# Optimization experiments

Hardware: AMD Instinct MI355X
Metric: run time of the kernel (lower is better)

Reference implementation:

```python
import jax, jax.numpy as jnp
import numpy as np
from jax import lax

CLIP = 5.0
LN_EPS = 1e-5


def _embed(feats, mean, std, W, b, g, beta):
    # InputNorm (eval mode, count>1): normalize with running stats, clamp.
    h = jnp.clip((feats - mean) / std, -CLIP, CLIP)
    h = lax.stop_gradient(h)  # torch runs InputNorm under no_grad
    # Linear + ReLU
    h = jax.nn.relu(h @ W + b)
    # LayerNorm over d_model
    mu = h.mean(-1, keepdims=True)
    var = ((h - mu) ** 2).mean(-1, keepdims=True)
    return (h - mu) / jnp.sqrt(var + LN_EPS) * g + beta


def setup_inputs() -> dict:
    key = jax.random.key(0)
    ks = jax.random.split(key, 8)
    nA, fA = 300000, 32
    nB, fB = 150000, 48
    d = 256
    B = 512
    inp = {
        "featsA": jax.random.normal(ks[0], (nA, fA), jnp.float32),
        "featsB": jax.random.normal(ks[1], (nB, fB), jnp.float32),
        "normA_mean": jnp.zeros((fA,), jnp.float32),
        "normA_std": jnp.ones((fA,), jnp.float32),
        "normB_mean": jnp.zeros((fB,), jnp.float32),
        "normB_std": jnp.ones((fB,), jnp.float32),
        "WA": jax.random.normal(ks[2], (fA, d), jnp.float32) / np.sqrt(fA),
        "bA": jnp.zeros((d,), jnp.float32),
        "lnA_g": jnp.ones((d,), jnp.float32),
        "lnA_b": jnp.zeros((d,), jnp.float32),
        "WB_": jax.random.normal(ks[3], (fB, d), jnp.float32) / np.sqrt(fB),
        "bB": jnp.zeros((d,), jnp.float32),
        "lnB_g": jnp.ones((d,), jnp.float32),
        "lnB_b": jnp.zeros((d,), jnp.float32),
        "Wback": jax.random.normal(ks[4], (d, d), jnp.float32) / np.sqrt(d),
        "bback": jnp.zeros((d,), jnp.float32),
        "Wv": jax.random.normal(ks[5], (d, 1), jnp.float32) / np.sqrt(d),
        "bv": jnp.zeros((1,), jnp.float32),
        "batch_index": jax.random.randint(ks[6], (nA + nB,), 0, B, jnp.int64)
        if jax.config.jax_enable_x64 else jax.random.randint(ks[6], (nA + nB,), 0, B, jnp.int32).astype(jnp.int32),
        "num_obs": B,
    }
    return inp


def reference(featsA, featsB, normA_mean, normA_std, normB_mean, normB_std,
              WA, bA, lnA_g, lnA_b, WB_, bB, lnB_g, lnB_b,
              Wback, bback, Wv, bv, batch_index, num_obs):
    # Per-entity-type embedding stacks, concatenated in entity-type order
    xA = _embed(featsA, normA_mean, normA_std, WA, bA, lnA_g, lnA_b)
    xB = _embed(featsB, normB_mean, normB_std, WB_, bB, lnB_g, lnB_b)
    x = jnp.concatenate([xA, xB], axis=0)          # [N, d]
    x = jax.nn.relu(x @ Wback + bback)              # backbone
    # torch_scatter mean pooling over observations
    sums = jax.ops.segment_sum(x, batch_index, num_segments=num_obs)
    counts = jax.ops.segment_sum(jnp.ones((x.shape[0],), x.dtype), batch_index,
                                 num_segments=num_obs)
    pooled = sums / jnp.maximum(counts, 1.0)[:, None]  # empty segments -> 0
    return pooled @ Wv + bv                          # [num_obs, 1]
```

## Files before the change

kernel.cpp:

```cpp
#include <hip/hip_runtime.h>

#define NSEG 512
#define NSPLIT 32

typedef __attribute__((ext_vector_type(8))) short short8;
typedef __attribute__((ext_vector_type(4))) short short4v;
typedef __attribute__((ext_vector_type(4))) float floatx4;

#define WS_WAT   0
#define WS_WBT2  16384
#define WS_W2GA  49152
#define WS_W2GB  180224
#define WS_C1A   311296
#define WS_C2A   312320
#define WS_C1B   313344
#define WS_C2B   314368
#define WS_INVA  315392
#define WS_INVB  315520
#define WS_VPART 315712
#define WS_CPART 381248

__device__ __forceinline__ short f2bf(float f) {
  unsigned u = __builtin_bit_cast(unsigned, f);
  u += 0x7FFFu + ((u >> 16) & 1u);
  return (short)(u >> 16);
}

__global__ void prep_kernel(const float* __restrict__ WA, const float* __restrict__ WB,
                            const float* __restrict__ Wback,
                            const float* __restrict__ gA, const float* __restrict__ betaA,
                            const float* __restrict__ gB, const float* __restrict__ betaB,
                            const float* __restrict__ bback,
                            const float* __restrict__ sA, const float* __restrict__ sB,
                            char* __restrict__ ws) {
  short* waT  = (short*)(ws + WS_WAT);
  short* wbT2 = (short*)(ws + WS_WBT2);
  short* w2gA = (short*)(ws + WS_W2GA);
  short* w2gB = (short*)(ws + WS_W2GB);
  float* c1A = (float*)(ws + WS_C1A);
  float* c2A = (float*)(ws + WS_C2A);
  float* c1B = (float*)(ws + WS_C1B);
  float* c2B = (float*)(ws + WS_C2B);
  float* invA = (float*)(ws + WS_INVA);
  float* invB = (float*)(ws + WS_INVB);
  float* vz   = (float*)(ws + WS_VPART);
  int tid = blockIdx.x * blockDim.x + threadIdx.x;
  int stride = gridDim.x * blockDim.x;
  for (int i = tid; i < 32*256; i += stride) {
    int n = i >> 5, k = i & 31;
    waT[i] = f2bf(WA[k*256 + n]);
  }
  for (int i = tid; i < 256*64; i += stride) {
    int n = i >> 6, k = i & 63;
    wbT2[i] = (k < 48) ? f2bf(WB[k*256 + n]) : (short)0;
  }
  for (int i = tid; i < 256*256; i += stride) {
    int n = i >> 8, k = i & 255;
    float w = Wback[k*256 + n];
    w2gA[i] = f2bf(gA[k] * w);
    w2gB[i] = f2bf(gB[k] * w);
  }
  if (blockIdx.x < 4 && threadIdx.x < 256) {
    int n = threadIdx.x;
    int which = blockIdx.x;
    const float* coef = (which == 0) ? gA : (which == 1) ? betaA : (which == 2) ? gB : betaB;
    float a = 0.f;
    #pragma unroll 8
    for (int k = 0; k < 256; k++) a = fmaf(coef[k], Wback[k*256 + n], a);
    if (which == 0)      c1A[n] = a;
    else if (which == 1) c2A[n] = a + bback[n];
    else if (which == 2) c1B[n] = a;
    else                 c2B[n] = a + bback[n];
  }
  if (tid < 32) invA[tid] = 1.0f / sA[tid];
  if (tid < 48) invB[tid] = 1.0f / sB[tid];
  for (int i = tid; i < 2*NSPLIT*NSEG; i += stride) vz[i] = 0.0f;
}

__global__ __launch_bounds__(256, 4) void fused_kernel(
    const float* __restrict__ featsA, const float* __restrict__ featsB,
    const float* __restrict__ mA, const float* __restrict__ mB,
    const float* __restrict__ bA, const float* __restrict__ bB,
    const float* __restrict__ Wv, const int* __restrict__ bidx,
    const char* __restrict__ ws, float* __restrict__ vpart, float* __restrict__ cpart,
    int tilesA, int nA, int nB)
{
  __shared__ __attribute__((aligned(16))) short ztile[64*264];
  __shared__ __attribute__((aligned(16))) float sred[64][4];
  __shared__ __attribute__((aligned(16))) float s2red[64][4];
  __shared__ __attribute__((aligned(16))) float vpw[64][4];

  const int tid  = threadIdx.x;
  const int wave = tid >> 6;
  const int lane = tid & 63;
  const int l15  = lane & 15;
  const int quad = lane >> 4;

  const bool isA = (blockIdx.x < (unsigned)tilesA);
  const int  tb  = isA ? blockIdx.x : (blockIdx.x - tilesA);
  const int  r0  = tb * 64;
  const int  nrows = isA ? nA : nB;
  const int  valid = min(64, nrows - r0);
  const float* feats = isA ? featsA : featsB;
  const float* meanp = isA ? mA : mB;
  const float* invp  = (const float*)(ws + (isA ? WS_INVA : WS_INVB));
  const float* biasp = isA ? bA : bB;
  const short* weT   = (const short*)(ws + (isA ? WS_WAT : WS_WBT2));
  const short* w2gT  = (const short*)(ws + (isA ? WS_W2GA : WS_W2GB));
  const float* c1p   = (const float*)(ws + (isA ? WS_C1A : WS_C1B));
  const float* c2p   = (const float*)(ws + (isA ? WS_C2A : WS_C2B));
  const int f       = isA ? 32 : 48;
  const int kstride = isA ? 32 : 64;
  const int ksteps  = isA ? 1 : 2;

  floatx4 acc1[4][4];
  #pragma unroll
  for (int mt = 0; mt < 4; mt++)
    #pragma unroll
    for (int nt = 0; nt < 4; nt++)
      acc1[mt][nt] = 0.0f;

  for (int kk = 0; kk < ksteps; kk++) {
    const int k0 = kk*32 + quad*8;
    const bool kvalid = (k0 < f);
    floatx4 mv0 = {0,0,0,0}, mv1 = {0,0,0,0}, iv0 = {1,1,1,1}, iv1 = {1,1,1,1};
    if (kvalid) {
      mv0 = *(const floatx4*)(meanp + k0);  mv1 = *(const floatx4*)(meanp + k0 + 4);
      iv0 = *(const floatx4*)(invp + k0);   iv1 = *(const floatx4*)(invp + k0 + 4);
    }
    short8 bfw[4];
    #pragma unroll
    for (int nt = 0; nt < 4; nt++)
      bfw[nt] = *(const short8*)(weT + (size_t)(64*wave + 16*nt + l15) * kstride + kk*32 + quad*8);
    #pragma unroll
    for (int mt = 0; mt < 4; mt++) {
      short8 a = {0,0,0,0,0,0,0,0};
      int row = 16*mt + l15;
      if (kvalid && row < valid) {
        const float* fp = feats + (size_t)(r0 + row) * f + k0;
        floatx4 x0 = *(const floatx4*)fp;
        floatx4 x1 = *(const floatx4*)(fp + 4);
        #pragma unroll
        for (int e = 0; e < 4; e++) {
          float h0 = (x0[e] - mv0[e]) * iv0[e];
          h0 = fminf(fmaxf(h0, -5.0f), 5.0f);
          a[e] = f2bf(h0);
          float h1 = (x1[e] - mv1[e]) * iv1[e];
          h1 = fminf(fmaxf(h1, -5.0f), 5.0f);
          a[4+e] = f2bf(h1);
        }
      }
      #pragma unroll
      for (int nt = 0; nt < 4; nt++)
        acc1[mt][nt] = __builtin_amdgcn_mfma_f32_16x16x32_bf16(bfw[nt], a, acc1[mt][nt], 0, 0, 0);
    }
  }

  float sacc[4], s2acc[4];
  #pragma unroll
  for (int mt = 0; mt < 4; mt++) { sacc[mt] = 0.f; s2acc[mt] = 0.f; }

  #pragma unroll
  for (int nt = 0; nt < 4; nt++) {
    const int c0 = 64*wave + 16*nt + 4*quad;
    floatx4 b1v = *(const floatx4*)(biasp + c0);
    #pragma unroll
    for (int mt = 0; mt < 4; mt++) {
      short4v pk;
      #pragma unroll
      for (int r = 0; r < 4; r++) {
        float h = fmaxf(acc1[mt][nt][r] + b1v[r], 0.0f);
        sacc[mt] += h;
        s2acc[mt] = fmaf(h, h, s2acc[mt]);
        pk[r] = f2bf(h);
      }
      *(short4v*)(ztile + (16*mt + l15)*264 + c0) = pk;
    }
  }
  #pragma unroll
  for (int mt = 0; mt < 4; mt++) {
    float s = sacc[mt], s2 = s2acc[mt];
    s += __shfl_xor(s, 16, 64);  s2 += __shfl_xor(s2, 16, 64);
    s += __shfl_xor(s, 32, 64);  s2 += __shfl_xor(s2, 32, 64);
    if (lane < 16) {
      sred[16*mt + lane][wave] = s;
      s2red[16*mt + lane][wave] = s2;
    }
  }
  __syncthreads();

  float rsv[4], mrsv[4];
  #pragma unroll
  for (int mt = 0; mt < 4; mt++) {
    int row = 16*mt + l15;
    floatx4 sv  = *(const floatx4*)sred[row];
    floatx4 s2v = *(const floatx4*)s2red[row];
    float s  = sv[0] + sv[1] + sv[2] + sv[3];
    float s2 = s2v[0] + s2v[1] + s2v[2] + s2v[3];
    float mu  = s * (1.0f/256.0f);
    float var = fmaxf(s2 * (1.0f/256.0f) - mu*mu, 0.0f);
    float rs  = rsqrtf(var + 1e-5f);
    rsv[mt]  = rs;
    mrsv[mt] = mu * rs;
  }

  floatx4 acc2[4][4];
  #pragma unroll
  for (int mt = 0; mt < 4; mt++)
    #pragma unroll
    for (int nt = 0; nt < 4; nt++)
      acc2[mt][nt] = 0.0f;

  #pragma unroll 2
  for (int kk = 0; kk < 8; kk++) {
    short8 bf[4];
    #pragma unroll
    for (int nt = 0; nt < 4; nt++)
      bf[nt] = *(const short8*)(w2gT + (size_t)(64*wave + 16*nt + l15)*256 + kk*32 + quad*8);
    #pragma unroll
    for (int mt = 0; mt < 4; mt++) {
      short8 a = *(const short8*)(ztile + (16*mt + l15)*264 + kk*32 + quad*8);
      #pragma unroll
      for (int nt = 0; nt < 4; nt++)
        acc2[mt][nt] = __builtin_amdgcn_mfma_f32_16x16x32_bf16(bf[nt], a, acc2[mt][nt], 0, 0, 0);
    }
  }

  float pv[4] = {0.f, 0.f, 0.f, 0.f};
  #pragma unroll
  for (int nt = 0; nt < 4; nt++) {
    const int c0 = 64*wave + 16*nt + 4*quad;
    floatx4 c1v = *(const floatx4*)(c1p + c0);
    floatx4 c2v = *(const floatx4*)(c2p + c0);
    floatx4 wvv = *(const floatx4*)(Wv + c0);
    #pragma unroll
    for (int mt = 0; mt < 4; mt++) {
      float rs = rsv[mt], mrs = mrsv[mt];
      #pragma unroll
      for (int r = 0; r < 4; r++) {
        float t = fmaf(-mrs, c1v[r], c2v[r]);
        float y = fmaf(rs, acc2[mt][nt][r], t);
        y = fmaxf(y, 0.0f);
        pv[mt] = fmaf(y, wvv[r], pv[mt]);
      }
    }
  }
  #pragma unroll
  for (int mt = 0; mt < 4; mt++) {
    float p = pv[mt];
    p += __shfl_xor(p, 16, 64);
    p += __shfl_xor(p, 32, 64);
    if (lane < 16) vpw[16*mt + lane][wave] = p;
  }
  __syncthreads();

  if (tid < valid) {
    floatx4 vv = *(const floatx4*)vpw[tid];
    float v = vv[0] + vv[1] + vv[2] + vv[3];
    int g = (isA ? r0 : (nA + r0)) + tid;
    int seg = bidx[g];
    int split = blockIdx.x & (NSPLIT - 1);
    atomicAdd(&vpart[split*NSEG + seg], v);
    atomicAdd(&cpart[split*NSEG + seg], 1.0f);
  }
}

__global__ void final_kernel(const float* __restrict__ vpart, const float* __restrict__ cpart,
                             const float* __restrict__ bv, float* __restrict__ out, int nseg) {
  int s = blockIdx.x * blockDim.x + threadIdx.x;
  if (s < nseg) {
    float a = 0.0f, c = 0.0f;
    #pragma unroll 8
    for (int i = 0; i < NSPLIT; i++) { a += vpart[i*NSEG + s]; c += cpart[i*NSEG + s]; }
    out[s] = a / fmaxf(c, 1.0f) + bv[0];
  }
}

extern "C" void kernel_launch(void* const* d_in, const int* in_sizes, int n_in,
                              void* d_out, int out_size, void* d_ws, size_t ws_size,
                              hipStream_t stream) {
  const float* featsA = (const float*)d_in[0];
  const float* featsB = (const float*)d_in[1];
  const float* mA     = (const float*)d_in[2];
  const float* sA     = (const float*)d_in[3];
  const float* mB     = (const float*)d_in[4];
  const float* sB     = (const float*)d_in[5];
  const float* WA     = (const float*)d_in[6];
  const float* bA     = (const float*)d_in[7];
  const float* gA     = (const float*)d_in[8];
  const float* betaA  = (const float*)d_in[9];
  const float* WB     = (const float*)d_in[10];
  const float* bB     = (const float*)d_in[11];
  const float* gB     = (const float*)d_in[12];
  const float* betaB  = (const float*)d_in[13];
  const float* Wback  = (const float*)d_in[14];
  const float* bback  = (const float*)d_in[15];
  const float* Wv     = (const float*)d_in[16];
  const float* bv     = (const float*)d_in[17];
  const int*   bidx   = (const int*)d_in[18];

  const int nA = in_sizes[0] / 32;
  const int nB = in_sizes[1] / 48;
  char* ws = (char*)d_ws;
  float* vpart = (float*)(ws + WS_VPART);
  float* cpart = (float*)(ws + WS_CPART);
  float* out = (float*)d_out;

  prep_kernel<<<256, 256, 0, stream>>>(WA, WB, Wback, gA, betaA, gB, betaB,
                                       bback, sA, sB, ws);

  const int tilesA = (nA + 63) / 64;
  const int tilesB = (nB + 63) / 64;
  fused_kernel<<<tilesA + tilesB, 256, 0, stream>>>(
      featsA, featsB, mA, mB, bA, bB, Wv, bidx, ws, vpart, cpart, tilesA, nA, nB);

  final_kernel<<<(out_size + 255) / 256, 256, 0, stream>>>(vpart, cpart, bv, out, out_size);
}
```

Baseline: 307.3 us.

## Pre-normalize input features to padded bf16 buffers in a separate kernel

Adds a norm_kernel that applies InputNorm (subtract mean, scale by inverse std, clamp) and converts features to bf16. It writes them into zero-padded row-major buffers in the workspace, with B padded to 64 columns. The fused kernel then loads ready bf16 MFMA operands with a single 16-byte load per tile, with no per-element normalization or bounds checks. This adds an extra kernel launch and an extra round trip through global memory for the features, and it only runs when the workspace is large enough.

```diff
diff --git a/kernel.cpp b/kernel.cpp
--- a/kernel.cpp
+++ b/kernel.cpp
@@ -19,6 +19,7 @@
 #define WS_INVB  315520
 #define WS_VPART 315712
 #define WS_CPART 381248
+#define WS_NF    446848
 
 __device__ __forceinline__ short f2bf(float f) {
   unsigned u = __builtin_bit_cast(unsigned, f);
@@ -46,6 +47,8 @@
   float* vz   = (float*)(ws + WS_VPART);
   int tid = blockIdx.x * blockDim.x + threadIdx.x;
   int stride = gridDim.x * blockDim.x;
+  if (tid < 32) invA[tid] = 1.0f / sA[tid];
+  if (tid < 48) invB[tid] = 1.0f / sB[tid];
   for (int i = tid; i < 32*256; i += stride) {
     int n = i >> 5, k = i & 31;
     waT[i] = f2bf(WA[k*256 + n]);
@@ -72,13 +75,68 @@
     else if (which == 2) c1B[n] = a;
     else                 c2B[n] = a + bback[n];
   }
-  if (tid < 32) invA[tid] = 1.0f / sA[tid];
-  if (tid < 48) invB[tid] = 1.0f / sB[tid];
   for (int i = tid; i < 2*NSPLIT*NSEG; i += stride) vz[i] = 0.0f;
 }
 
+__global__ __launch_bounds__(256) void norm_kernel(
+    const float* __restrict__ fA, const float* __restrict__ fB,
+    const float* __restrict__ mA, const float* __restrict__ mB,
+    const char* __restrict__ ws, short* __restrict__ nfA, short* __restrict__ nfB,
+    int rowsApad, int nA, int rowsBpad, int nB)
+{
+  const float* invA = (const float*)(ws + WS_INVA);
+  const float* invB = (const float*)(ws + WS_INVB);
+  int tid = blockIdx.x * blockDim.x + threadIdx.x;
+  int stride = gridDim.x * blockDim.x;
+  int chunksA = rowsApad * 4;
+  int chunksB = rowsBpad * 8;
+  for (int i = tid; i < chunksA + chunksB; i += stride) {
+    short8 o = {0,0,0,0,0,0,0,0};
+    if (i < chunksA) {
+      int row = i >> 2, c0 = (i & 3) * 8;
+      if (row < nA) {
+        const float* fp = fA + (size_t)row*32 + c0;
+        floatx4 x0 = *(const floatx4*)fp;
+        floatx4 x1 = *(const floatx4*)(fp + 4);
+        floatx4 mv0 = *(const floatx4*)(mA + c0);
+        floatx4 mv1 = *(const floatx4*)(mA + c0 + 4);
+        floatx4 iv0 = *(const floatx4*)(invA + c0);
+        floatx4 iv1 = *(const floatx4*)(invA + c0 + 4);
+        #pragma unroll
+        for (int e = 0; e < 4; e++) {
+          float h0 = fminf(fmaxf((x0[e] - mv0[e]) * iv0[e], -5.0f), 5.0f);
+          float h1 = fminf(fmaxf((x1[e] - mv1[e]) * iv1[e], -5.0f), 5.0f);
+          o[e] = f2bf(h0);  o[4+e] = f2bf(h1);
+        }
+      }
+      *(short8*)(nfA + (size_t)row*32 + c0) = o;
+    } else {
+      int j = i - chunksA;
+      int row = j >> 3, c0 = (j & 7) * 8;
+      if (row < nB && c0 < 48) {
+        const float* fp = fB + (size_t)row*48 + c0;
+        floatx4 x0 = *(const floatx4*)fp;
+        floatx4 x1 = *(const floatx4*)(fp + 4);
+        floatx4 mv0 = *(const floatx4*)(mB + c0);
+        floatx4 mv1 = *(const floatx4*)(mB + c0 + 4);
+        floatx4 iv0 = *(const floatx4*)(invB + c0);
+        floatx4 iv1 = *(const floatx4*)(invB + c0 + 4);
+        #pragma unroll
+        for (int e = 0; e < 4; e++) {
+          float h0 = fminf(fmaxf((x0[e] - mv0[e]) * iv0[e], -5.0f), 5.0f);
+          float h1 = fminf(fmaxf((x1[e] - mv1[e]) * iv1[e], -5.0f), 5.0f);
+          o[e] = f2bf(h0);  o[4+e] = f2bf(h1);
+        }
+      }
+      *(short8*)(nfB + (size_t)row*64 + c0) = o;
+    }
+  }
+}
+
+template <bool PRE>
 __global__ __launch_bounds__(256, 4) void fused_kernel(
     const float* __restrict__ featsA, const float* __restrict__ featsB,
+    const short* __restrict__ nfA, const short* __restrict__ nfB,
     const float* __restrict__ mA, const float* __restrict__ mB,
     const float* __restrict__ bA, const float* __restrict__ bB,
     const float* __restrict__ Wv, const int* __restrict__ bidx,
@@ -102,6 +160,7 @@
   const int  nrows = isA ? nA : nB;
   const int  valid = min(64, nrows - r0);
   const float* feats = isA ? featsA : featsB;
+  const short* nf    = isA ? nfA : nfB;
   const float* meanp = isA ? mA : mB;
   const float* invp  = (const float*)(ws + (isA ? WS_INVA : WS_INVB));
   const float* biasp = isA ? bA : bB;
@@ -121,38 +180,49 @@
       acc1[mt][nt] = 0.0f;
 
   for (int kk = 0; kk < ksteps; kk++) {
-    const int k0 = kk*32 + quad*8;
-    const bool kvalid = (k0 < f);
-    floatx4 mv0 = {0,0,0,0}, mv1 = {0,0,0,0}, iv0 = {1,1,1,1}, iv1 = {1,1,1,1};
-    if (kvalid) {
-      mv0 = *(const floatx4*)(meanp + k0);  mv1 = *(const floatx4*)(meanp + k0 + 4);
-      iv0 = *(const floatx4*)(invp + k0);   iv1 = *(const floatx4*)(invp + k0 + 4);
-    }
     short8 bfw[4];
     #pragma unroll
     for (int nt = 0; nt < 4; nt++)
       bfw[nt] = *(const short8*)(weT + (size_t)(64*wave + 16*nt + l15) * kstride + kk*32 + quad*8);
-    #pragma unroll
-    for (int mt = 0; mt < 4; mt++) {
-      short8 a = {0,0,0,0,0,0,0,0};
-      int row = 16*mt + l15;
-      if (kvalid && row < valid) {
-        const float* fp = feats + (size_t)(r0 + row) * f + k0;
-        floatx4 x0 = *(const floatx4*)fp;
-        floatx4 x1 = *(const floatx4*)(fp + 4);
+
+    if (PRE) {
+      #pragma unroll
+      for (int mt = 0; mt < 4; mt++) {
+        short8 a = *(const short8*)(nf + (size_t)(r0 + 16*mt + l15) * kstride + kk*32 + quad*8);
         #pragma unroll
-        for (int e = 0; e < 4; e++) {
-          float h0 = (x0[e] - mv0[e]) * iv0[e];
-          h0 = fminf(fmaxf(h0, -5.0f), 5.0f);
-          a[e] = f2bf(h0);
-          float h1 = (x1[e] - mv1[e]) * iv1[e];
-          h1 = fminf(fmaxf(h1, -5.0f), 5.0f);
-          a[4+e] = f2bf(h1);
+        for (int nt = 0; nt < 4; nt++)
+          acc1[mt][nt] = __builtin_amdgcn_mfma_f32_16x16x32_bf16(bfw[nt], a, acc1[mt][nt], 0, 0, 0);
+      }
+    } else {
+      const int k0 = kk*32 + quad*8;
+      const bool kvalid = (k0 < f);
+      floatx4 mv0 = {0,0,0,0}, mv1 = {0,0,0,0}, iv0 = {1,1,1,1}, iv1 = {1,1,1,1};
+      if (kvalid) {
+        mv0 = *(const floatx4*)(meanp + k0);  mv1 = *(const floatx4*)(meanp + k0 + 4);
+        iv0 = *(const floatx4*)(invp + k0);   iv1 = *(const floatx4*)(invp + k0 + 4);
+      }
+      #pragma unroll
+      for (int mt = 0; mt < 4; mt++) {
+        short8 a = {0,0,0,0,0,0,0,0};
+        int row = 16*mt + l15;
+        if (kvalid && row < valid) {
+          const float* fp = feats + (size_t)(r0 + row) * f + k0;
+          floatx4 x0 = *(const floatx4*)fp;
+          floatx4 x1 = *(const floatx4*)(fp + 4);
+          #pragma unroll
+          for (int e = 0; e < 4; e++) {
+            float h0 = (x0[e] - mv0[e]) * iv0[e];
+            h0 = fminf(fmaxf(h0, -5.0f), 5.0f);
+            a[e] = f2bf(h0);
+            float h1 = (x1[e] - mv1[e]) * iv1[e];
+            h1 = fminf(fmaxf(h1, -5.0f), 5.0f);
+            a[4+e] = f2bf(h1);
+          }
         }
-      }
-      #pragma unroll
-      for (int nt = 0; nt < 4; nt++)
-        acc1[mt][nt] = __builtin_amdgcn_mfma_f32_16x16x32_bf16(bfw[nt], a, acc1[mt][nt], 0, 0, 0);
+        #pragma unroll
+        for (int nt = 0; nt < 4; nt++)
+          acc1[mt][nt] = __builtin_amdgcn_mfma_f32_16x16x32_bf16(bfw[nt], a, acc1[mt][nt], 0, 0, 0);
+      }
     }
   }
 
@@ -306,13 +376,35 @@
   float* cpart = (float*)(ws + WS_CPART);
   float* out = (float*)d_out;
 
+  const int tilesA = (nA + 63) / 64;
+  const int tilesB = (nB + 63) / 64;
+  const int rowsApad = tilesA * 64;
+  const int rowsBpad = tilesB * 64;
+  const size_t nfa_off = WS_NF;
+  const size_t nfb_off = nfa_off + (size_t)rowsApad * 32 * 2;
+  const size_t ws_need = nfb_off + (size_t)rowsBpad * 64 * 2;
+  const bool pre = (ws_size >= ws_need);
+  short* nfA = (short*)(ws + nfa_off);
+  short* nfB = (short*)(ws + nfb_off);
+
   prep_kernel<<<256, 256, 0, stream>>>(WA, WB, Wback, gA, betaA, gB, betaB,
                                        bback, sA, sB, ws);
 
-  const int tilesA = (nA + 63) / 64;
-  const int tilesB = (nB + 63) / 64;
-  fused_kernel<<<tilesA + tilesB, 256, 0, stream>>>(
-      featsA, featsB, mA, mB, bA, bB, Wv, bidx, ws, vpart, cpart, tilesA, nA, nB);
-
-  final_kernel<<<(out_size + 255) / 256, 256, 0, stream>>>(vpart, cpart, bv, out, out_size);
-}
+  if (pre) {
+    const int chunks = rowsApad * 4 + rowsBpad * 8;
+    int nblk = (chunks + 255) / 256;
+    if (nblk > 2048) nblk = 2048;
+    norm_kernel<<<nblk, 256, 0, stream>>>(featsA, featsB, mA, mB, ws, nfA, nfB,
+                                          rowsApad, nA, rowsBpad, nB);
+    fused_kernel<true><<<tilesA + tilesB, 256, 0, stream>>>(
+        featsA, featsB, nfA, nfB, mA, mB, bA, bB, Wv, bidx, ws, vpart, cpart,
+        tilesA, nA, nB);
+  } else {
+    fused_kernel<false><<<tilesA + tilesB, 256, 0, stream>>>(
+        featsA, featsB, nfA, nfB, mA, mB, bA, bB, Wv, bidx, ws, vpart, cpart,
+        tilesA, nA, nB);
+  }
+
+  if (out_size > 0)
+    final_kernel<<<(out_size + 255) / 256, 256, 0, stream>>>(vpart, cpart, bv, out, out_size);
+}
```

Measured after the change: 309.0 us. Within noise of the previous version (+0.6%).
